# Performance work log

Measured on AMD Instinct MI355X. Metric: run time of the kernel, lower is better.

## Reference

```python
import jax, jax.numpy as jnp
import numpy as np

TAU = 2.0      # LIF membrane time constant
VTH = 1.0      # spike threshold (spikingjelly default)
T = 10         # time steps

@jax.custom_vjp
def spike(v):
    return (v >= VTH).astype(v.dtype)

def _spike_fwd(v):
    return spike(v), v

def _spike_bwd(v, g):
    # spikingjelly surrogate.Sigmoid(alpha=4.0)
    alpha = 4.0
    s = jax.nn.sigmoid(alpha * (v - VTH))
    return (g * alpha * s * (1.0 - s),)

spike.defvjp(_spike_fwd, _spike_bwd)

def lif(v, c):
    # charge: v += (x - v)/tau with v_reset = 0
    v = v + (c - v) / TAU
    s = spike(v)
    v = v * (1.0 - s)  # hard reset to 0 where spiked
    return v, s

def setup_inputs() -> dict:
    key = jax.random.key(0)
    ks = jax.random.split(key, 7)
    B, D, H, O = 1024, 4000, 2048, 1000
    x = jax.random.normal(ks[0], (B, D), jnp.float32)
    W1 = jax.random.normal(ks[1], (D, H), jnp.float32) / jnp.sqrt(D)
    b1 = jax.random.normal(ks[2], (H,), jnp.float32) * 0.01
    W2 = jax.random.normal(ks[3], (H, H), jnp.float32) / jnp.sqrt(H)
    b2 = jax.random.normal(ks[4], (H,), jnp.float32) * 0.01
    W3 = jax.random.normal(ks[5], (H, O), jnp.float32) / jnp.sqrt(H)
    b3 = jax.random.normal(ks[6], (O,), jnp.float32) * 0.01
    return {"x": x, "W1": W1, "b1": b1, "W2": W2, "b2": b2, "W3": W3, "b3": b3}

def reference(x, W1, b1, W2, b2, W3, b3):
    B, D = x.shape
    H = W1.shape[1]
    O = W3.shape[1]
    chunk = D // T
    # accumulated_input at step t equals x with columns >= end_idx zeroed
    ends = ((jnp.arange(T) + 1) * chunk).at[-1].set(D)          # [T]
    masks = (jnp.arange(D)[None, :] < ends[:, None]).astype(x.dtype)  # [T, D]

    def step(carry, mask):
        v1, v2, v3 = carry
        xt = x * mask                       # accumulated (prefix-filled) input
        v1, s1 = lif(v1, xt @ W1 + b1)
        v2, s2 = lif(v2, s1 @ W2 + b2)
        v3, s3 = lif(v3, s2 @ W3 + b3)
        return (v1, v2, v3), s3

    init = (jnp.zeros((B, H), x.dtype), jnp.zeros((B, H), x.dtype), jnp.zeros((B, O), x.dtype))
    _, outs = jax.lax.scan(step, init, masks)
    return outs[-1]  # module returns outputs[-1], shape [B, O]
```

## Files before the change

kernel.cpp:

```cpp
#include <hip/hip_runtime.h>
#include <hip/hip_bf16.h>


typedef _Float16 half8 __attribute__((ext_vector_type(8)));
typedef __attribute__((ext_vector_type(4))) float f32x4;
typedef __attribute__((ext_vector_type(4))) unsigned short us4;

#ifndef __has_builtin
#define __has_builtin(x) 0
#endif
#if __has_builtin(__builtin_amdgcn_global_load_lds)
#define HAS_GLLDS 1
#else
#define HAS_GLLDS 0
#endif

template<int MODE>
__global__ __launch_bounds__(256)
void gemm_planes(const _Float16* __restrict__ A, size_t aStride, int lda,
                 const _Float16* __restrict__ B, size_t bStride, int ldb,
                 int K, int kChunk, float scale,
                 float* __restrict__ C, int Npad, int ls)
{
    constexpr int NA = MODE ? 2 : 1;
    constexpr int NB = 2;
    constexpr int FM = MODE ? 4 : 8;
    constexpr int FN = MODE ? 4 : 2;

    __shared__ __align__(16) char tiles[(NA + NB) * 8192];

    const int tid = threadIdx.x;
    const int b   = blockIdx.x;
    const int xcd = b & 7, ii = b >> 3;
    const int ntp = 1 << ls;
    const int n_tile = xcd * ntp + (ii & (ntp - 1));
    const int m_tile = ii >> ls;
    const int m0 = m_tile * 128, n0 = n_tile * 128;

    const int t     = MODE ? (m0 >> 10) : 0;
    const int kbase = MODE ? t * kChunk : 0;
    const int arow0 = MODE ? (m0 & 1023) : m0;

    int srow[2], schk[2];
    #pragma unroll
    for (int h = 0; h < 2; ++h) {
        const int s   = h * 256 + tid;
        const int sub = s >> 8, sp = s & 255;
        const int ss  = sp >> 3, gg = ((sp & 7) - ss) & 7;
        srow[h] = sub * 64 + 2 * ss + (gg >> 2);
        schk[h] = gg & 3;
    }
    const int wbase = (tid & ~63) * 16;

    const _Float16* srcA[NA][2];
    const _Float16* srcB[NB][2];
    #pragma unroll
    for (int p = 0; p < NA; ++p)
        #pragma unroll
        for (int h = 0; h < 2; ++h)
            srcA[p][h] = A + p * aStride + (size_t)(arow0 + srow[h]) * lda
                           + kbase + schk[h] * 8;
    #pragma unroll
    for (int q = 0; q < NB; ++q)
        #pragma unroll
        for (int h = 0; h < 2; ++h)
            srcB[q][h] = B + q * bStride + (size_t)(n0 + srow[h]) * ldb
                           + kbase + schk[h] * 8;

    const int lane = tid & 63, w = tid >> 6;
    const int wm = MODE ? ((w >> 1) * 64) : 0;
    const int wn = MODE ? ((w & 1) * 64) : (w * 32);
    const int lm = lane & 15, ck = lane >> 4;

    int aOff[FM], bOff[FN];
    #pragma unroll
    for (int i = 0; i < FM; ++i) {
        const int r = wm + i * 16 + lm, sub = r >> 6, rr = r & 63, s2 = rr >> 1;
        aOff[i] = sub * 4096 + (s2 * 8 + ((((rr & 1) << 2) + ck + s2) & 7)) * 16;
    }
    #pragma unroll
    for (int j = 0; j < FN; ++j) {
        const int r = wn + j * 16 + lm, sub = r >> 6, rr = r & 63, s2 = rr >> 1;
        bOff[j] = sub * 4096 + (s2 * 8 + ((((rr & 1) << 2) + ck + s2) & 7)) * 16;
    }

    f32x4 acc[FM][FN] = {};

    const int nIter = K / 32;
    for (int it = 0; it < nIter; ++it) {
        const int kk = it * 32;
        #pragma unroll
        for (int p = 0; p < NA; ++p) {
            #pragma unroll
            for (int h = 0; h < 2; ++h) {
#if HAS_GLLDS
                __builtin_amdgcn_global_load_lds(
                    (const __attribute__((address_space(1))) void*)(srcA[p][h] + kk),
                    (__attribute__((address_space(3))) void*)(tiles + p * 8192 + h * 4096 + wbase),
                    16, 0, 0);
#else
                *(float4*)(tiles + p * 8192 + (h * 256 + tid) * 16) =
                    *(const float4*)(srcA[p][h] + kk);
#endif
            }
        }
        #pragma unroll
        for (int q = 0; q < NB; ++q) {
            #pragma unroll
            for (int h = 0; h < 2; ++h) {
#if HAS_GLLDS
                __builtin_amdgcn_global_load_lds(
                    (const __attribute__((address_space(1))) void*)(srcB[q][h] + kk),
                    (__attribute__((address_space(3))) void*)(tiles + (NA + q) * 8192 + h * 4096 + wbase),
                    16, 0, 0);
#else
                *(float4*)(tiles + (NA + q) * 8192 + (h * 256 + tid) * 16) =
                    *(const float4*)(srcB[q][h] + kk);
#endif
            }
        }
        __syncthreads();

        half8 aF[NA][FM], bF[NB][FN];
        #pragma unroll
        for (int p = 0; p < NA; ++p)
            #pragma unroll
            for (int i = 0; i < FM; ++i)
                aF[p][i] = *(const half8*)(tiles + p * 8192 + aOff[i]);
        #pragma unroll
        for (int q = 0; q < NB; ++q)
            #pragma unroll
            for (int j = 0; j < FN; ++j)
                bF[q][j] = *(const half8*)(tiles + (NA + q) * 8192 + bOff[j]);

        if (MODE == 0) {
            #pragma unroll
            for (int q = 0; q < 2; ++q)
                #pragma unroll
                for (int i = 0; i < FM; ++i)
                    #pragma unroll
                    for (int j = 0; j < FN; ++j)
                        acc[i][j] = __builtin_amdgcn_mfma_f32_16x16x32_f16(
                            aF[0][i], bF[q][j], acc[i][j], 0, 0, 0);
        } else {
            constexpr int PA[3] = {0,0,1}, PB[3] = {0,1,0};
            #pragma unroll
            for (int pp = 0; pp < 3; ++pp)
                #pragma unroll
                for (int i = 0; i < FM; ++i)
                    #pragma unroll
                    for (int j = 0; j < FN; ++j)
                        acc[i][j] = __builtin_amdgcn_mfma_f32_16x16x32_f16(
                            aF[PA[pp] % NA][i], bF[PB[pp]][j], acc[i][j], 0, 0, 0);
        }
        __syncthreads();
    }

    const int rq = ck * 4;
    #pragma unroll
    for (int i = 0; i < FM; ++i) {
        #pragma unroll
        for (int j = 0; j < FN; ++j) {
            const int n = n0 + wn + j * 16 + lm;
            #pragma unroll
            for (int r = 0; r < 4; ++r) {
                const int m = m0 + wm + i * 16 + rq + r;
                C[(size_t)m * Npad + n] = acc[i][j][r] * scale;
            }
        }
    }
}

__global__ __launch_bounds__(256)
void lif_scan(const float* __restrict__ C, const float* __restrict__ bias,
              unsigned short* __restrict__ sout,
              float* __restrict__ fout,
              int Hpad, int Nreal, int prefix)
{
    const int W4 = Hpad >> 2;
    const int idx = blockIdx.x * 256 + threadIdx.x;
    if (idx >= (W4 << 10)) return;
    const int bb = idx / W4, n4 = idx - bb * W4;
    const float4 b4 = *(const float4*)(bias + n4 * 4);
    const float bs[4] = {b4.x, b4.y, b4.z, b4.w};
    float v[4] = {0.f,0.f,0.f,0.f}, c[4] = {0.f,0.f,0.f,0.f};
    for (int t = 0; t < 10; ++t) {
        const size_t row = (size_t)((t << 10) + bb);
        const float4 p4 = *(const float4*)(C + row * Hpad + n4 * 4);
        const float pv[4] = {p4.x, p4.y, p4.z, p4.w};
        float sv[4];
        #pragma unroll
        for (int e = 0; e < 4; ++e) {
            c[e] = prefix ? (c[e] + pv[e]) : pv[e];
            const float vv = (v[e] + (c[e] + bs[e])) * 0.5f;
            const float sp = (vv >= 1.0f) ? 1.0f : 0.0f;
            v[e] = (sp != 0.0f) ? 0.0f : vv;
            sv[e] = sp;
        }
        if (sout) {
            us4 o;
            #pragma unroll
            for (int e = 0; e < 4; ++e) o[e] = (sv[e] != 0.0f) ? 0x3C00 : 0;
            *(us4*)(sout + row * Hpad + n4 * 4) = o;
        }
        if (fout && t == 9) {
            #pragma unroll
            for (int e = 0; e < 4; ++e) {
                const int n = n4 * 4 + e;
                if (n < Nreal) fout[(size_t)bb * Nreal + n] = sv[e];
            }
        }
    }
}

__device__ __forceinline__ void f16split2(float val, _Float16& hi, _Float16& mid) {
    const float vs = val * 256.0f;
    hi = (_Float16)vs;
    mid = (_Float16)(vs - (float)hi);
}

__global__ __launch_bounds__(256)
void split2_t(const float* __restrict__ W, int K, int Nreal, int Npad,
              _Float16* __restrict__ out)
{
    __shared__ float tl[32][33];
    const int k0 = blockIdx.x * 32, n0 = blockIdx.y * 32;
    const int tx = threadIdx.x & 31, ty = threadIdx.x >> 5;
    #pragma unroll
    for (int i = 0; i < 4; ++i) {
        const int k = k0 + ty + i * 8, n = n0 + tx;
        tl[ty + i * 8][tx] = (n < Nreal) ? W[(size_t)k * Nreal + n] : 0.f;
    }
    __syncthreads();
    const size_t plane = (size_t)Npad * K;
    #pragma unroll
    for (int i = 0; i < 4; ++i) {
        const int n = n0 + ty + i * 8, k = k0 + tx;
        _Float16 hi, mid;
        f16split2(tl[tx][ty + i * 8], hi, mid);
        const size_t idx = (size_t)n * K + k;
        out[idx] = hi; out[plane + idx] = mid;
    }
}

__global__ __launch_bounds__(256)
void split2_w1(const float* __restrict__ W1, _Float16* __restrict__ out)
{
    __shared__ float tl[32][33];
    const int kk0 = blockIdx.x * 32, n0 = blockIdx.y * 32;
    const int tx = threadIdx.x & 31, ty = threadIdx.x >> 5;
    #pragma unroll
    for (int i = 0; i < 4; ++i) {
        const int kk = kk0 + ty + i * 8;
        const int tt = kk / 416, j = kk - tt * 416;
        tl[ty + i * 8][tx] = (j < 400) ? W1[(size_t)(tt * 400 + j) * 2048 + (n0 + tx)] : 0.f;
    }
    __syncthreads();
    const size_t plane = (size_t)2048 * 4160;
    #pragma unroll
    for (int i = 0; i < 4; ++i) {
        const int n = n0 + ty + i * 8, kk = kk0 + tx;
        _Float16 hi, mid;
        f16split2(tl[tx][ty + i * 8], hi, mid);
        const size_t idx = (size_t)n * 4160 + kk;
        out[idx] = hi; out[plane + idx] = mid;
    }
}

__global__ __launch_bounds__(256)
void splitx(const float* __restrict__ x, _Float16* __restrict__ out)
{
    const int id = blockIdx.x * 256 + threadIdx.x;
    if (id >= 1024 * 4160) return;
    const int m = id / 4160, kk = id - m * 4160;
    const int tt = kk / 416, j = kk - tt * 416;
    const float val = (j < 400) ? x[(size_t)m * 4000 + tt * 400 + j] : 0.f;
    const size_t PS = (size_t)1024 * 4160;
    _Float16 hi, mid;
    f16split2(val, hi, mid);
    out[id] = hi; out[PS + id] = mid;
}

__global__ __launch_bounds__(256)
void gemm_lif_f32fb(const float* __restrict__ A, int lda,
                    const float* __restrict__ B, int ldb,
                    const float* __restrict__ bias,
                    float* __restrict__ cacc, float* __restrict__ v,
                    float* __restrict__ s, int M, int N, int K)
{
    __shared__ float As[16][68];
    __shared__ float Bs[16][68];
    const int tid = threadIdx.x;
    const int tx = tid & 15, ty = tid >> 4;
    const int row0 = blockIdx.y * 64, col0 = blockIdx.x * 64;
    const int am = tid >> 2, ak = (tid & 3) * 4;
    const int bk = tid >> 4, bn = (tid & 15) * 4;
    float acc[4][4];
    #pragma unroll
    for (int i = 0; i < 4; ++i)
        #pragma unroll
        for (int j = 0; j < 4; ++j) acc[i][j] = 0.f;
    for (int k0 = 0; k0 < K; k0 += 16) {
        const float4 a4 = *(const float4*)(A + (size_t)(row0 + am) * lda + (k0 + ak));
        As[ak + 0][am] = a4.x; As[ak + 1][am] = a4.y;
        As[ak + 2][am] = a4.z; As[ak + 3][am] = a4.w;
        {
            const int col = col0 + bn;
            const float* bp = B + (size_t)(k0 + bk) * ldb + col;
            float4 b4;
            if (col + 3 < N) b4 = *(const float4*)bp;
            else {
                b4.x = (col + 0 < N) ? bp[0] : 0.f;
                b4.y = (col + 1 < N) ? bp[1] : 0.f;
                b4.z = (col + 2 < N) ? bp[2] : 0.f;
                b4.w = 0.f;
            }
            *(float4*)&Bs[bk][bn] = b4;
        }
        __syncthreads();
        #pragma unroll
        for (int kk = 0; kk < 16; ++kk) {
            float af[4], bf[4];
            #pragma unroll
            for (int i = 0; i < 4; ++i) af[i] = As[kk][ty * 4 + i];
            #pragma unroll
            for (int j = 0; j < 4; ++j) bf[j] = Bs[kk][tx * 4 + j];
            #pragma unroll
            for (int i = 0; i < 4; ++i)
                #pragma unroll
                for (int j = 0; j < 4; ++j) acc[i][j] += af[i] * bf[j];
        }
        __syncthreads();
    }
    #pragma unroll
    for (int i = 0; i < 4; ++i) {
        const int r = row0 + ty * 4 + i;
        #pragma unroll
        for (int j = 0; j < 4; ++j) {
            const int cidx = col0 + tx * 4 + j;
            if (cidx >= N) continue;
            const size_t idx = (size_t)r * N + cidx;
            float dot = acc[i][j];
            if (cacc) { dot += cacc[idx]; cacc[idx] = dot; }
            const float ch = dot + bias[cidx];
            const float vv = (v[idx] + ch) * 0.5f;
            const float sp = (vv >= 1.0f) ? 1.0f : 0.0f;
            v[idx] = (sp != 0.0f) ? 0.0f : vv;
            s[idx] = sp;
        }
    }
}

extern "C" void kernel_launch(void* const* d_in, const int* in_sizes, int n_in,
                              void* d_out, int out_size, void* d_ws, size_t ws_size,
                              hipStream_t stream) {
    const float* x  = (const float*)d_in[0];
    const float* W1 = (const float*)d_in[1];
    const float* b1 = (const float*)d_in[2];
    const float* W2 = (const float*)d_in[3];
    const float* b2 = (const float*)d_in[4];
    const float* W3 = (const float*)d_in[5];
    const float* b3 = (const float*)d_in[6];
    float* out = (float*)d_out;

    const int Bb = 1024, D = 4000, H = 2048, O = 1000, Op = 1024, T = 10;
    const int KP = 4160, CHP = 416, CH = 400;
    const int MS = T * Bb;
    const float SC1 = 1.0f / 65536.0f;
    const float SC23 = 1.0f / 256.0f;

    char* base = (char*)d_ws;
    _Float16* w2s = (_Float16*)(base);
    _Float16* w3s = (_Float16*)(base + 16777216);
    float*    b3p = (float*)(base + 25165824);
    _Float16* s1  = (_Float16*)(base + 25169920);
    float*    P   = (float*)(base + 67112960);
    _Float16* xs  = (_Float16*)(base + 150999040);
    _Float16* w1s = (_Float16*)(base + 168038400);
    _Float16* s2  = xs;
    float*    C3  = (float*)s1;
    const size_t need = 202117120;

    if (ws_size < need) {
        const size_t BH = (size_t)Bb * H, BO = (size_t)Bb * O;
        float* ws = (float*)d_ws;
        float* c1 = ws;        float* v1 = c1 + BH;  float* s1f = v1 + BH;
        float* v2 = s1f + BH;  float* s2f = v2 + BH; float* v3 = s2f + BH;
        hipMemsetAsync(d_ws, 0, (5 * BH + BO) * sizeof(float), stream);
        const dim3 blk(256);
        for (int t = 0; t < T; ++t) {
            gemm_lif_f32fb<<<dim3(H / 64, Bb / 64), blk, 0, stream>>>(
                x + t * CH, D, W1 + (size_t)t * CH * H, H, b1, c1, v1, s1f, Bb, H, CH);
            gemm_lif_f32fb<<<dim3(H / 64, Bb / 64), blk, 0, stream>>>(
                s1f, H, W2, H, b2, nullptr, v2, s2f, Bb, H, H);
            gemm_lif_f32fb<<<dim3((O + 63) / 64, Bb / 64), blk, 0, stream>>>(
                s2f, H, W3, O, b3, nullptr, v3, out, Bb, O, H);
        }
        return;
    }

    hipMemsetAsync(b3p, 0, 4096, stream);
    hipMemcpyAsync(b3p, b3, O * sizeof(float), hipMemcpyDeviceToDevice, stream);
    split2_t<<<dim3(H / 32, H / 32), 256, 0, stream>>>(W2, H, H, H, w2s);
    split2_t<<<dim3(H / 32, Op / 32), 256, 0, stream>>>(W3, H, O, Op, w3s);
    split2_w1<<<dim3(KP / 32, H / 32), 256, 0, stream>>>(W1, w1s);
    splitx<<<dim3((Bb * KP + 255) / 256), 256, 0, stream>>>(x, xs);

    const size_t PSx  = (size_t)Bb * KP;
    const size_t PSw1 = (size_t)H * KP;
    const size_t PSw2 = (size_t)H * H;
    const size_t PSw3 = (size_t)Op * H;

    gemm_planes<1><<<(MS / 128) * (H / 128), 256, 0, stream>>>(
        xs, PSx, KP, w1s, PSw1, KP, CHP, CHP, SC1, P, H, 1);
    lif_scan<<<(Bb * (H / 4) + 255) / 256, 256, 0, stream>>>(
        P, b1, (unsigned short*)s1, nullptr, H, H, 1);
    gemm_planes<0><<<(MS / 128) * (H / 128), 256, 0, stream>>>(
        s1, 0, H, w2s, PSw2, H, H, 0, SC23, P, H, 1);
    lif_scan<<<(Bb * (H / 4) + 255) / 256, 256, 0, stream>>>(
        P, b2, (unsigned short*)s2, nullptr, H, H, 0);
    gemm_planes<0><<<(MS / 128) * (Op / 128), 256, 0, stream>>>(
        s2, 0, H, w3s, PSw3, H, H, 0, SC23, C3, Op, 0);
    lif_scan<<<(Bb * (Op / 4) + 255) / 256, 256, 0, stream>>>(
        C3, b3p, nullptr, out, Op, O, 0);
}
```

Baseline: 523.2 us.

## Use int8 MFMA with three-digit weight planes for spike GEMMs

```diff
diff --git a/kernel.cpp b/kernel.cpp
--- a/kernel.cpp
+++ b/kernel.cpp
@@ -1,10 +1,11 @@
 #include <hip/hip_runtime.h>
 #include <hip/hip_bf16.h>
+#include <math.h>
 
 
 typedef _Float16 half8 __attribute__((ext_vector_type(8)));
 typedef __attribute__((ext_vector_type(4))) float f32x4;
-typedef __attribute__((ext_vector_type(4))) unsigned short us4;
+typedef __attribute__((ext_vector_type(4))) int i32x4;
 
 #ifndef __has_builtin
 #define __has_builtin(x) 0
@@ -15,19 +16,130 @@
 #define HAS_GLLDS 0
 #endif
 
-template<int MODE>
-__global__ __launch_bounds__(256)
-void gemm_planes(const _Float16* __restrict__ A, size_t aStride, int lda,
+__device__ __forceinline__ int swz(int r, int c) {
+    const int s2 = r >> 1;
+    return s2 * 8 + ((((r & 1) << 2) + c + s2) & 7);
+}
+
+__global__ __launch_bounds__(256, 3)
+void gemm_i8(const signed char* __restrict__ A, int lda,
+             const signed char* __restrict__ Bd, size_t bStride, int ldb,
+             int K, const unsigned* __restrict__ maxbits,
+             float* __restrict__ C, int Npad, int ls)
+{
+    __shared__ __align__(16) char tiles[5 * 4096];
+
+    const int tid = threadIdx.x;
+    const int b   = blockIdx.x;
+    const int xcd = b & 7, ii = b >> 3;
+    const int ntp = 1 << ls;
+    const int n_tile = xcd * ntp + (ii & (ntp - 1));
+    const int m_tile = ii >> ls;
+    const int m0 = m_tile * 128, n0 = n_tile * 64;
+
+    const int ss = tid >> 3;
+    const int gg = ((tid & 7) - ss) & 7;
+    const int rdec = 2 * ss + (gg >> 2);
+    const int cdec = gg & 3;
+    const int wbase = (tid & ~63) * 16;
+
+    const signed char* srcA0 = A + (size_t)(m0 + rdec) * lda + cdec * 16;
+    const signed char* srcA1 = A + (size_t)(m0 + 64 + rdec) * lda + cdec * 16;
+    const signed char* srcB[3];
+    #pragma unroll
+    for (int q = 0; q < 3; ++q)
+        srcB[q] = Bd + q * bStride + (size_t)(n0 + rdec) * ldb + cdec * 16;
+
+    const int lane = tid & 63, w = tid >> 6;
+    const int wm = (w >> 1) * 64, wn = (w & 1) * 32;
+    const int lm = lane & 15, ck = lane >> 4;
+
+    int aOff[4], bOff[2];
+    #pragma unroll
+    for (int i = 0; i < 4; ++i) {
+        const int r = wm + i * 16 + lm;
+        aOff[i] = (r >> 6) * 4096 + swz(r & 63, ck) * 16;
+    }
+    #pragma unroll
+    for (int j = 0; j < 2; ++j) {
+        const int r = wn + j * 16 + lm;
+        bOff[j] = 8192 + swz(r, ck) * 16;
+    }
+
+    i32x4 acc0[4][2] = {}, acc1[4][2] = {}, acc2[4][2] = {};
+
+    const int nIter = K / 64;
+    for (int it = 0; it < nIter; ++it) {
+        const int kk = it * 64;
+#if HAS_GLLDS
+        __builtin_amdgcn_global_load_lds(
+            (const __attribute__((address_space(1))) void*)(srcA0 + kk),
+            (__attribute__((address_space(3))) void*)(tiles + wbase), 16, 0, 0);
+        __builtin_amdgcn_global_load_lds(
+            (const __attribute__((address_space(1))) void*)(srcA1 + kk),
+            (__attribute__((address_space(3))) void*)(tiles + 4096 + wbase), 16, 0, 0);
+        #pragma unroll
+        for (int q = 0; q < 3; ++q)
+            __builtin_amdgcn_global_load_lds(
+                (const __attribute__((address_space(1))) void*)(srcB[q] + kk),
+                (__attribute__((address_space(3))) void*)(tiles + 8192 + q * 4096 + wbase),
+                16, 0, 0);
+#else
+        *(float4*)(tiles + tid * 16) = *(const float4*)(srcA0 + kk);
+        *(float4*)(tiles + 4096 + tid * 16) = *(const float4*)(srcA1 + kk);
+        #pragma unroll
+        for (int q = 0; q < 3; ++q)
+            *(float4*)(tiles + 8192 + q * 4096 + tid * 16) = *(const float4*)(srcB[q] + kk);
+#endif
+        __syncthreads();
+
+        i32x4 aF[4], bF[3][2];
+        #pragma unroll
+        for (int i = 0; i < 4; ++i) aF[i] = *(const i32x4*)(tiles + aOff[i]);
+        #pragma unroll
+        for (int q = 0; q < 3; ++q)
+            #pragma unroll
+            for (int j = 0; j < 2; ++j)
+                bF[q][j] = *(const i32x4*)(tiles + q * 4096 + bOff[j]);
+
+        #pragma unroll
+        for (int i = 0; i < 4; ++i)
+            #pragma unroll
+            for (int j = 0; j < 2; ++j) {
+                acc0[i][j] = __builtin_amdgcn_mfma_i32_16x16x64_i8(aF[i], bF[0][j], acc0[i][j], 0, 0, 0);
+                acc1[i][j] = __builtin_amdgcn_mfma_i32_16x16x64_i8(aF[i], bF[1][j], acc1[i][j], 0, 0, 0);
+                acc2[i][j] = __builtin_amdgcn_mfma_i32_16x16x64_i8(aF[i], bF[2][j], acc2[i][j], 0, 0, 0);
+            }
+        __syncthreads();
+    }
+
+    const int sexp = 21 - ilogbf(__uint_as_float(*maxbits));
+    const float sc = ldexpf(1.0f, -sexp);
+    const int rq = ck * 4;
+    #pragma unroll
+    for (int i = 0; i < 4; ++i) {
+        #pragma unroll
+        for (int j = 0; j < 2; ++j) {
+            const int n = n0 + wn + j * 16 + lm;
+            #pragma unroll
+            for (int r = 0; r < 4; ++r) {
+                const int m = m0 + wm + i * 16 + rq + r;
+                const long long v = ((long long)acc0[i][j][r] << 16) +
+                                    ((long long)acc1[i][j][r] << 8) +
+                                    (long long)acc2[i][j][r];
+                __builtin_nontemporal_store((float)v * sc, &C[(size_t)m * Npad + n]);
+            }
+        }
+    }
+}
+
+__global__ __launch_bounds__(256)
+void gemm_f16_l1(const _Float16* __restrict__ A, size_t aStride, int lda,
                  const _Float16* __restrict__ B, size_t bStride, int ldb,
                  int K, int kChunk, float scale,
                  float* __restrict__ C, int Npad, int ls)
 {
-    constexpr int NA = MODE ? 2 : 1;
-    constexpr int NB = 2;
-    constexpr int FM = MODE ? 4 : 8;
-    constexpr int FN = MODE ? 4 : 2;
-
-    __shared__ __align__(16) char tiles[(NA + NB) * 8192];
+    __shared__ __align__(16) char tiles[4 * 8192];
 
     const int tid = threadIdx.x;
     const int b   = blockIdx.x;
@@ -37,9 +149,9 @@
     const int m_tile = ii >> ls;
     const int m0 = m_tile * 128, n0 = n_tile * 128;
 
-    const int t     = MODE ? (m0 >> 10) : 0;
-    const int kbase = MODE ? t * kChunk : 0;
-    const int arow0 = MODE ? (m0 & 1023) : m0;
+    const int t     = m0 >> 10;
+    const int kbase = t * kChunk;
+    const int arow0 = m0 & 1023;
 
     int srow[2], schk[2];
     #pragma unroll
@@ -52,45 +164,36 @@
     }
     const int wbase = (tid & ~63) * 16;
 
-    const _Float16* srcA[NA][2];
-    const _Float16* srcB[NB][2];
-    #pragma unroll
-    for (int p = 0; p < NA; ++p)
-        #pragma unroll
-        for (int h = 0; h < 2; ++h)
-            srcA[p][h] = A + p * aStride + (size_t)(arow0 + srow[h]) * lda
-                           + kbase + schk[h] * 8;
-    #pragma unroll
-    for (int q = 0; q < NB; ++q)
-        #pragma unroll
-        for (int h = 0; h < 2; ++h)
-            srcB[q][h] = B + q * bStride + (size_t)(n0 + srow[h]) * ldb
-                           + kbase + schk[h] * 8;
+    const _Float16* srcA[2][2];
+    const _Float16* srcB[2][2];
+    #pragma unroll
+    for (int p = 0; p < 2; ++p)
+        #pragma unroll
+        for (int h = 0; h < 2; ++h) {
+            srcA[p][h] = A + p * aStride + (size_t)(arow0 + srow[h]) * lda + kbase + schk[h] * 8;
+            srcB[p][h] = B + p * bStride + (size_t)(n0 + srow[h]) * ldb + kbase + schk[h] * 8;
+        }
 
     const int lane = tid & 63, w = tid >> 6;
-    const int wm = MODE ? ((w >> 1) * 64) : 0;
-    const int wn = MODE ? ((w & 1) * 64) : (w * 32);
+    const int wm = (w >> 1) * 64, wn = (w & 1) * 64;
     const int lm = lane & 15, ck = lane >> 4;
 
-    int aOff[FM], bOff[FN];
-    #pragma unroll
-    for (int i = 0; i < FM; ++i) {
-        const int r = wm + i * 16 + lm, sub = r >> 6, rr = r & 63, s2 = rr >> 1;
-        aOff[i] = sub * 4096 + (s2 * 8 + ((((rr & 1) << 2) + ck + s2) & 7)) * 16;
-    }
-    #pragma unroll
-    for (int j = 0; j < FN; ++j) {
-        const int r = wn + j * 16 + lm, sub = r >> 6, rr = r & 63, s2 = rr >> 1;
-        bOff[j] = sub * 4096 + (s2 * 8 + ((((rr & 1) << 2) + ck + s2) & 7)) * 16;
-    }
-
-    f32x4 acc[FM][FN] = {};
+    int aOff[4], bOff[4];
+    #pragma unroll
+    for (int i = 0; i < 4; ++i) {
+        const int r = wm + i * 16 + lm;
+        aOff[i] = (r >> 6) * 4096 + swz(r & 63, ck) * 16;
+        const int r2 = wn + i * 16 + lm;
+        bOff[i] = (r2 >> 6) * 4096 + swz(r2 & 63, ck) * 16;
+    }
+
+    f32x4 acc[4][4] = {};
 
     const int nIter = K / 32;
     for (int it = 0; it < nIter; ++it) {
         const int kk = it * 32;
         #pragma unroll
-        for (int p = 0; p < NA; ++p) {
+        for (int p = 0; p < 2; ++p)
             #pragma unroll
             for (int h = 0; h < 2; ++h) {
 #if HAS_GLLDS
@@ -98,82 +201,55 @@
                     (const __attribute__((address_space(1))) void*)(srcA[p][h] + kk),
                     (__attribute__((address_space(3))) void*)(tiles + p * 8192 + h * 4096 + wbase),
                     16, 0, 0);
-#else
-                *(float4*)(tiles + p * 8192 + (h * 256 + tid) * 16) =
-                    *(const float4*)(srcA[p][h] + kk);
-#endif
-            }
-        }
-        #pragma unroll
-        for (int q = 0; q < NB; ++q) {
-            #pragma unroll
-            for (int h = 0; h < 2; ++h) {
-#if HAS_GLLDS
                 __builtin_amdgcn_global_load_lds(
-                    (const __attribute__((address_space(1))) void*)(srcB[q][h] + kk),
-                    (__attribute__((address_space(3))) void*)(tiles + (NA + q) * 8192 + h * 4096 + wbase),
+                    (const __attribute__((address_space(1))) void*)(srcB[p][h] + kk),
+                    (__attribute__((address_space(3))) void*)(tiles + (2 + p) * 8192 + h * 4096 + wbase),
                     16, 0, 0);
 #else
-                *(float4*)(tiles + (NA + q) * 8192 + (h * 256 + tid) * 16) =
-                    *(const float4*)(srcB[q][h] + kk);
+                *(float4*)(tiles + p * 8192 + (h * 256 + tid) * 16) = *(const float4*)(srcA[p][h] + kk);
+                *(float4*)(tiles + (2 + p) * 8192 + (h * 256 + tid) * 16) = *(const float4*)(srcB[p][h] + kk);
 #endif
             }
-        }
         __syncthreads();
 
-        half8 aF[NA][FM], bF[NB][FN];
-        #pragma unroll
-        for (int p = 0; p < NA; ++p)
-            #pragma unroll
-            for (int i = 0; i < FM; ++i)
+        half8 aF[2][4], bF[2][4];
+        #pragma unroll
+        for (int p = 0; p < 2; ++p)
+            #pragma unroll
+            for (int i = 0; i < 4; ++i) {
                 aF[p][i] = *(const half8*)(tiles + p * 8192 + aOff[i]);
-        #pragma unroll
-        for (int q = 0; q < NB; ++q)
-            #pragma unroll
-            for (int j = 0; j < FN; ++j)
-                bF[q][j] = *(const half8*)(tiles + (NA + q) * 8192 + bOff[j]);
-
-        if (MODE == 0) {
-            #pragma unroll
-            for (int q = 0; q < 2; ++q)
+                bF[p][i] = *(const half8*)(tiles + (2 + p) * 8192 + bOff[i]);
+            }
+
+        constexpr int PA[3] = {0,0,1}, PB[3] = {0,1,0};
+        #pragma unroll
+        for (int pp = 0; pp < 3; ++pp)
+            #pragma unroll
+            for (int i = 0; i < 4; ++i)
                 #pragma unroll
-                for (int i = 0; i < FM; ++i)
-                    #pragma unroll
-                    for (int j = 0; j < FN; ++j)
-                        acc[i][j] = __builtin_amdgcn_mfma_f32_16x16x32_f16(
-                            aF[0][i], bF[q][j], acc[i][j], 0, 0, 0);
-        } else {
-            constexpr int PA[3] = {0,0,1}, PB[3] = {0,1,0};
-            #pragma unroll
-            for (int pp = 0; pp < 3; ++pp)
-                #pragma unroll
-                for (int i = 0; i < FM; ++i)
-                    #pragma unroll
-                    for (int j = 0; j < FN; ++j)
-                        acc[i][j] = __builtin_amdgcn_mfma_f32_16x16x32_f16(
-                            aF[PA[pp] % NA][i], bF[PB[pp]][j], acc[i][j], 0, 0, 0);
-        }
+                for (int j = 0; j < 4; ++j)
+                    acc[i][j] = __builtin_amdgcn_mfma_f32_16x16x32_f16(
+                        aF[PA[pp]][i], bF[PB[pp]][j], acc[i][j], 0, 0, 0);
         __syncthreads();
     }
 
     const int rq = ck * 4;
     #pragma unroll
-    for (int i = 0; i < FM; ++i) {
-        #pragma unroll
-        for (int j = 0; j < FN; ++j) {
+    for (int i = 0; i < 4; ++i)
+        #pragma unroll
+        for (int j = 0; j < 4; ++j) {
             const int n = n0 + wn + j * 16 + lm;
             #pragma unroll
             for (int r = 0; r < 4; ++r) {
                 const int m = m0 + wm + i * 16 + rq + r;
-                C[(size_t)m * Npad + n] = acc[i][j][r] * scale;
-            }
-        }
-    }
+                __builtin_nontemporal_store(acc[i][j][r] * scale, &C[(size_t)m * Npad + n]);
+            }
+        }
 }
 
 __global__ __launch_bounds__(256)
 void lif_scan(const float* __restrict__ C, const float* __restrict__ bias,
-              unsigned short* __restrict__ sout,
+              signed char* __restrict__ sout,
               float* __restrict__ fout,
               int Hpad, int Nreal, int prefix)
 {
@@ -186,22 +262,21 @@
     float v[4] = {0.f,0.f,0.f,0.f}, c[4] = {0.f,0.f,0.f,0.f};
     for (int t = 0; t < 10; ++t) {
         const size_t row = (size_t)((t << 10) + bb);
-        const float4 p4 = *(const float4*)(C + row * Hpad + n4 * 4);
-        const float pv[4] = {p4.x, p4.y, p4.z, p4.w};
+        const f32x4 p4 = __builtin_nontemporal_load((const f32x4*)(C + row * Hpad + n4 * 4));
         float sv[4];
         #pragma unroll
         for (int e = 0; e < 4; ++e) {
-            c[e] = prefix ? (c[e] + pv[e]) : pv[e];
+            c[e] = prefix ? (c[e] + p4[e]) : p4[e];
             const float vv = (v[e] + (c[e] + bs[e])) * 0.5f;
             const float sp = (vv >= 1.0f) ? 1.0f : 0.0f;
             v[e] = (sp != 0.0f) ? 0.0f : vv;
             sv[e] = sp;
         }
         if (sout) {
-            us4 o;
-            #pragma unroll
-            for (int e = 0; e < 4; ++e) o[e] = (sv[e] != 0.0f) ? 0x3C00 : 0;
-            *(us4*)(sout + row * Hpad + n4 * 4) = o;
+            unsigned pack = 0;
+            #pragma unroll
+            for (int e = 0; e < 4; ++e) pack |= (sv[e] != 0.0f ? 1u : 0u) << (8 * e);
+            *(unsigned*)(sout + row * Hpad + n4 * 4) = pack;
         }
         if (fout && t == 9) {
             #pragma unroll
@@ -210,6 +285,47 @@
                 if (n < Nreal) fout[(size_t)bb * Nreal + n] = sv[e];
             }
         }
+    }
+}
+
+__global__ __launch_bounds__(256)
+void maxabs_kern(const float* __restrict__ w, int n, unsigned* __restrict__ out)
+{
+    float m = 0.f;
+    for (int i = blockIdx.x * 256 + threadIdx.x; i < n; i += gridDim.x * 256)
+        m = fmaxf(m, fabsf(w[i]));
+    #pragma unroll
+    for (int off = 32; off > 0; off >>= 1)
+        m = fmaxf(m, __shfl_down(m, off, 64));
+    if ((threadIdx.x & 63) == 0) atomicMax(out, __float_as_uint(m));
+}
+
+__global__ __launch_bounds__(256)
+void dsplit_t(const float* __restrict__ W, int K, int Nreal, int Npad,
+              signed char* __restrict__ out, const unsigned* __restrict__ maxbits)
+{
+    __shared__ float tl[32][33];
+    const int sexp = 21 - ilogbf(__uint_as_float(*maxbits));
+    const float fs = ldexpf(1.0f, sexp);
+    const int k0 = blockIdx.x * 32, n0 = blockIdx.y * 32;
+    const int tx = threadIdx.x & 31, ty = threadIdx.x >> 5;
+    #pragma unroll
+    for (int i = 0; i < 4; ++i) {
+        const int k = k0 + ty + i * 8, n = n0 + tx;
+        tl[ty + i * 8][tx] = (n < Nreal) ? W[(size_t)k * Nreal + n] : 0.f;
+    }
+    __syncthreads();
+    const size_t plane = (size_t)Npad * K;
+    #pragma unroll
+    for (int i = 0; i < 4; ++i) {
+        const int n = n0 + ty + i * 8, k = k0 + tx;
+        int wi = (int)lrintf(tl[tx][ty + i * 8] * fs);
+        const int d0 = ((wi + 128) & 255) - 128; wi = (wi - d0) >> 8;
+        const int d1 = ((wi + 128) & 255) - 128; wi = (wi - d1) >> 8;
+        const size_t idx = (size_t)n * K + k;
+        out[idx]             = (signed char)wi;
+        out[plane + idx]     = (signed char)d1;
+        out[2 * plane + idx] = (signed char)d0;
     }
 }
 
@@ -217,30 +333,6 @@
     const float vs = val * 256.0f;
     hi = (_Float16)vs;
     mid = (_Float16)(vs - (float)hi);
-}
-
-__global__ __launch_bounds__(256)
-void split2_t(const float* __restrict__ W, int K, int Nreal, int Npad,
-              _Float16* __restrict__ out)
-{
-    __shared__ float tl[32][33];
-    const int k0 = blockIdx.x * 32, n0 = blockIdx.y * 32;
-    const int tx = threadIdx.x & 31, ty = threadIdx.x >> 5;
-    #pragma unroll
-    for (int i = 0; i < 4; ++i) {
-        const int k = k0 + ty + i * 8, n = n0 + tx;
-        tl[ty + i * 8][tx] = (n < Nreal) ? W[(size_t)k * Nreal + n] : 0.f;
-    }
-    __syncthreads();
-    const size_t plane = (size_t)Npad * K;
-    #pragma unroll
-    for (int i = 0; i < 4; ++i) {
-        const int n = n0 + ty + i * 8, k = k0 + tx;
-        _Float16 hi, mid;
-        f16split2(tl[tx][ty + i * 8], hi, mid);
-        const size_t idx = (size_t)n * K + k;
-        out[idx] = hi; out[plane + idx] = mid;
-    }
 }
 
 __global__ __launch_bounds__(256)
@@ -367,19 +459,19 @@
     const int KP = 4160, CHP = 416, CH = 400;
     const int MS = T * Bb;
     const float SC1 = 1.0f / 65536.0f;
-    const float SC23 = 1.0f / 256.0f;
 
     char* base = (char*)d_ws;
-    _Float16* w2s = (_Float16*)(base);
-    _Float16* w3s = (_Float16*)(base + 16777216);
-    float*    b3p = (float*)(base + 25165824);
-    _Float16* s1  = (_Float16*)(base + 25169920);
-    float*    P   = (float*)(base + 67112960);
-    _Float16* xs  = (_Float16*)(base + 150999040);
-    _Float16* w1s = (_Float16*)(base + 168038400);
-    _Float16* s2  = xs;
-    float*    C3  = (float*)s1;
-    const size_t need = 202117120;
+    unsigned*    hdr = (unsigned*)(base);
+    float*       b3p = (float*)(base + 4096);
+    signed char* w2d = (signed char*)(base + 8192);
+    signed char* w3d = (signed char*)(base + 12591104);
+    signed char* s1  = (signed char*)(base + 18882560);
+    signed char* s2  = (signed char*)(base + 39854080);
+    float*       P   = (float*)(base + 60825600);
+    _Float16*    xs  = (_Float16*)(base + 144711680);
+    _Float16*    w1s = (_Float16*)(base + 161751040);
+    float*       C3  = P;
+    const size_t need = 195829760;
 
     if (ws_size < need) {
         const size_t BH = (size_t)Bb * H, BO = (size_t)Bb * O;
@@ -399,28 +491,28 @@
         return;
     }
 
-    hipMemsetAsync(b3p, 0, 4096, stream);
+    hipMemsetAsync(base, 0, 8192, stream);
     hipMemcpyAsync(b3p, b3, O * sizeof(float), hipMemcpyDeviceToDevice, stream);
-    split2_t<<<dim3(H / 32, H / 32), 256, 0, stream>>>(W2, H, H, H, w2s);
-    split2_t<<<dim3(H / 32, Op / 32), 256, 0, stream>>>(W3, H, O, Op, w3s);
+    maxabs_kern<<<512, 256, 0, stream>>>(W2, H * H, hdr + 0);
+    maxabs_kern<<<512, 256, 0, stream>>>(W3, H * O, hdr + 1);
+    dsplit_t<<<dim3(H / 32, H / 32), 256, 0, stream>>>(W2, H, H, H, w2d, hdr + 0);
+    dsplit_t<<<dim3(H / 32, Op / 32), 256, 0, stream>>>(W3, H, O, Op, w3d, hdr + 1);
     split2_w1<<<dim3(KP / 32, H / 32), 256, 0, stream>>>(W1, w1s);
     splitx<<<dim3((Bb * KP + 255) / 256), 256, 0, stream>>>(x, xs);
 
     const size_t PSx  = (size_t)Bb * KP;
     const size_t PSw1 = (size_t)H * KP;
-    const size_t PSw2 = (size_t)H * H;
-    const size_t PSw3 = (size_t)Op * H;
-
-    gemm_planes<1><<<(MS / 128) * (H / 128), 256, 0, stream>>>(
+
+    gemm_f16_l1<<<(MS / 128) * (H / 128), 256, 0, stream>>>(
         xs, PSx, KP, w1s, PSw1, KP, CHP, CHP, SC1, P, H, 1);
     lif_scan<<<(Bb * (H / 4) + 255) / 256, 256, 0, stream>>>(
-        P, b1, (unsigned short*)s1, nullptr, H, H, 1);
-    gemm_planes<0><<<(MS / 128) * (H / 128), 256, 0, stream>>>(
-        s1, 0, H, w2s, PSw2, H, H, 0, SC23, P, H, 1);
+        P, b1, s1, nullptr, H, H, 1);
+    gemm_i8<<<(MS / 128) * (H / 64), 256, 0, stream>>>(
+        s1, H, w2d, (size_t)H * H, H, H, hdr + 0, P, H, 2);
     lif_scan<<<(Bb * (H / 4) + 255) / 256, 256, 0, stream>>>(
-        P, b2, (unsigned short*)s2, nullptr, H, H, 0);
-    gemm_planes<0><<<(MS / 128) * (Op / 128), 256, 0, stream>>>(
-        s2, 0, H, w3s, PSw3, H, H, 0, SC23, C3, Op, 0);
+        P, b2, s2, nullptr, H, H, 0);
+    gemm_i8<<<(MS / 128) * (Op / 64), 256, 0, stream>>>(
+        s2, H, w3d, (size_t)Op * H, H, H, hdr + 1, C3, Op, 1);
     lif_scan<<<(Bb * (Op / 4) + 255) / 256, 256, 0, stream>>>(
         C3, b3p, nullptr, out, Op, O, 0);
 }
```

Measured after the change: 524.5 us. About the same (+0.2%).
